# Optimization experiments

Hardware: AMD Instinct MI355X
Metric: run time of the kernel (lower is better)

Reference implementation:

```python
import jax, jax.numpy as jnp
import numpy as np

B, T, D, N = 32, 512, 1024, 1024


def setup_inputs() -> dict:
    key = jax.random.key(0)
    k1, k2, k3, k4, k5 = jax.random.split(key, 5)
    x = jax.random.normal(k1, (B, T, D), dtype=jnp.float32)
    h0 = jnp.zeros((B, N), dtype=jnp.float32)  # self.h Variable init
    # GRUCell params: gate kernel [D+N, 2N], candidate kernel [D+N, N]
    Wg = jax.random.normal(k2, (D + N, 2 * N), dtype=jnp.float32) * 0.05
    bg = jax.random.normal(k3, (2 * N,), dtype=jnp.float32) * 0.05 + 1.0  # TF gate bias init 1.0
    Wc = jax.random.normal(k4, (D + N, N), dtype=jnp.float32) * 0.05
    bc = jax.random.normal(k5, (N,), dtype=jnp.float32) * 0.05
    return {"x": x, "h0": h0, "Wg": Wg, "bg": bg, "Wc": Wc, "bc": bc}


def reference(x, h0, Wg, bg, Wc, bc):
    # tf.nn.rnn_cell.GRUCell recurrence via dynamic_rnn, single layer
    def step(h, x_t):
        xh = jnp.concatenate([x_t, h], axis=-1)           # [B, D+N]
        gates = jax.nn.sigmoid(xh @ Wg + bg)              # [B, 2N]
        r, u = jnp.split(gates, 2, axis=-1)
        xrh = jnp.concatenate([x_t, r * h], axis=-1)      # [B, D+N]
        c = jnp.tanh(xrh @ Wc + bc)                       # [B, N]
        h_new = u * h + (1.0 - u) * c
        return h_new, h_new

    xs = jnp.swapaxes(x, 0, 1)                            # [T, B, D]
    _, outs = jax.lax.scan(step, h0, xs)                  # outs: [T, B, N]
    outputs = jnp.swapaxes(outs, 0, 1)                    # [B, T, N]
    activations = outputs.reshape(-1, N)                  # [B*T, N]
    return activations
```

## Files before the change

### kernel.cpp

```cpp
#include <hip/hip_runtime.h>
#include <hip/hip_bf16.h>

#define B_ 32
#define T_ 512
#define D_ 1024
#define N_ 1024
#define NWG 192
#define NGATE 128
#define TPB 256
#define SMEM_BYTES (131072 + 8192 + 64 + 2112)

typedef __attribute__((ext_vector_type(8))) short short8v;
typedef __attribute__((ext_vector_type(4))) float f32x4;

__device__ __forceinline__ float bf2f(unsigned short u) {
  union { float f; unsigned int i; } c; c.i = ((unsigned int)u) << 16; return c.f;
}
__device__ __forceinline__ unsigned short f2bf(float f) {
  union { float f; unsigned int i; } c; c.f = f;
  unsigned int r = c.i + 0x7FFFu + ((c.i >> 16) & 1u);
  return (unsigned short)(r >> 16);
}
__device__ __forceinline__ unsigned cvtpk(float a, float b) {
  unsigned r;
  asm("v_cvt_pk_bf16_f32 %0, %1, %2" : "=v"(r) : "v"(a), "v"(b));
  return r;
}
__device__ __forceinline__ short8v pack_frag(f32x4 lo, f32x4 hi) {
  union { unsigned u[4]; short8v s; } c;
  c.u[0] = cvtpk(lo[0], lo[1]); c.u[1] = cvtpk(lo[2], lo[3]);
  c.u[2] = cvtpk(hi[0], hi[1]); c.u[3] = cvtpk(hi[2], hi[3]);
  return c.s;
}

__device__ __forceinline__ void st_bf16_sc(unsigned short* p, unsigned short v) {
  asm volatile("global_store_short %0, %1, off sc0 sc1"
               :: "v"((unsigned long long)p), "v"((unsigned)v) : "memory");
}
__device__ __forceinline__ void st_f32_sc(float* p, float v) {
  asm volatile("global_store_dword %0, %1, off sc0 sc1"
               :: "v"((unsigned long long)p), "v"(v) : "memory");
}

__device__ __forceinline__ void flag_store(unsigned* line, unsigned v) {
  __hip_atomic_store(line, v, __ATOMIC_RELAXED, __HIP_MEMORY_SCOPE_AGENT);
}
__device__ __forceinline__ void poll_pred(const unsigned* p, bool act, unsigned tgt) {
  int tries = 0;
  for (;;) {
    unsigned v = tgt;
    if (act) v = __hip_atomic_load(p, __ATOMIC_RELAXED, __HIP_MEMORY_SCOPE_AGENT);
    if (__all((int)(v >= tgt))) break;
    __builtin_amdgcn_s_sleep(1);
    if (++tries > (1 << 20)) break;
  }
}

__device__ __forceinline__ int frag_off(int m, int k) {
  const int mt = m >> 4, ks = k >> 5, kk = k & 31;
  const int l = (m & 15) + (((kk >> 2) & 3) << 4);
  const int j = (kk & 3) + ((kk >> 4) << 2);
  return ((mt * 32 + ks) * 64 + l) * 8 + j;
}

template <int KS>
__device__ __forceinline__ void build_xfrags(const float* __restrict__ x, int t,
                                             int kbase, int lane,
                                             short8v frag[2][KS]) {
#pragma unroll
  for (int mt = 0; mt < 2; ++mt) {
    const int m = mt * 16 + (lane & 15);
    const float* row = x + ((size_t)m * T_ + t) * D_;
#pragma unroll
    for (int ks = 0; ks < KS; ++ks) {
      const int k0 = kbase + ks * 32 + ((lane >> 4) << 2);
      f32x4 lo = *(const f32x4*)(row + k0);
      f32x4 hi = *(const f32x4*)(row + k0 + 16);
      frag[mt][ks] = pack_frag(lo, hi);
    }
  }
}

template <int KS>
__device__ __forceinline__ void mfma_reg(const short8v frag[2][KS],
                                         const unsigned short* __restrict__ ldsW,
                                         int ksg0, f32x4* acc, int lane) {
#pragma unroll
  for (int mt = 0; mt < 2; ++mt)
#pragma unroll
    for (int ks = 0; ks < KS; ++ks) {
      const int ksg = ksg0 + ks;
      short8v bhi = *(const short8v*)(ldsW + ((size_t)(0 * 64 + ksg) * 64 + lane) * 8);
      short8v blo = *(const short8v*)(ldsW + ((size_t)(1 * 64 + ksg) * 64 + lane) * 8);
      acc[mt] = __builtin_amdgcn_mfma_f32_16x16x32_bf16(frag[mt][ks], bhi, acc[mt], 0, 0, 0);
      acc[mt] = __builtin_amdgcn_mfma_f32_16x16x32_bf16(frag[mt][ks], blo, acc[mt], 0, 0, 0);
    }
}

__global__ __launch_bounds__(TPB, 1) void gru_persistent(
    const float* __restrict__ x, const float* __restrict__ h0,
    const float* __restrict__ Wg, const float* __restrict__ bg,
    const float* __restrict__ Wc, const float* __restrict__ bc,
    float* __restrict__ out,
    unsigned* __restrict__ ctrs,
    unsigned short* __restrict__ hq,
    unsigned short* __restrict__ rhq,
    float* __restrict__ u_buf,
    float* __restrict__ h_buf)
{
  const int wg = blockIdx.x;
  const int tid = threadIdx.x;
  const int lane = tid & 63;
  const int wv = tid >> 6;

  extern __shared__ char smem[];
  unsigned short* ldsW = (unsigned short*)smem;
  float* ldsR = (float*)(smem + 131072);
  float* ldsBias = (float*)(smem + 131072 + 8192);
  float* ldsH = (float*)(smem + 131072 + 8192 + 64);

  unsigned* flagH = ctrs;
  unsigned* flagG = ctrs + 64 * 16;

  const bool is_gate = wg < NGATE;
  const int c0 = (is_gate ? wg : (wg - NGATE)) * 16;
  const float* Wsrc = is_gate ? Wg : Wc;
  const int ldw = is_gate ? 2 * N_ : N_;
  const float* bias = is_gate ? bg : bc;

  const int col = tid & 15, row = tid >> 4;
  const int colg = c0 + col;
  const int b0 = row, b1 = 16 + row;

  for (int i = tid; i < 64 * 64; i += TPB) {
    const int ks = i >> 6, l = i & 63;
    const int n = l & 15, kqp = (l >> 4) * 4;
#pragma unroll
    for (int j = 0; j < 8; ++j) {
      const int k = ks * 32 + ((j < 4) ? 0 : 16) + kqp + (j & 3);
      const float w = Wsrc[(size_t)k * ldw + c0 + n];
      const unsigned short hi = f2bf(w);
      const unsigned short lo = f2bf(w - bf2f(hi));
      ldsW[((size_t)(0 * 64 + ks) * 64 + l) * 8 + j] = hi;
      ldsW[((size_t)(1 * 64 + ks) * 64 + l) * 8 + j] = lo;
    }
  }
  if (tid < 16) ldsBias[tid] = bias[c0 + tid];
  __syncthreads();

  if (is_gate) {
    const bool r_wg = (c0 < N_);
    unsigned* myflag = flagG + (size_t)wg * 16;
    const unsigned* pollp = nullptr; bool pact = false;
    if (lane < 16)                { pollp = flagH + (size_t)(16 * wv + lane) * 16; pact = true; }
    else if (lane == 16 && r_wg)  { pollp = flagH + (size_t)wg * 16;               pact = true; }

    f32x4 accA[2] = {{0.f,0.f,0.f,0.f},{0.f,0.f,0.f,0.f}};
    {
      short8v xf[2][8];
      build_xfrags<8>(x, 0, wv * 256, lane, xf);
      mfma_reg<8>(xf, ldsW, wv * 8, accA, lane);
    }
    for (int t = 0; t < T_; ++t) {
      poll_pred(pollp, pact, (unsigned)(t + 1));
      f32x4 hvec = {0.f,0.f,0.f,0.f};
      const bool do_h = r_wg && (tid < 128);
      if (do_h) {
        const float* hsrc = h_buf + (size_t)(c0 + (tid & 15)) * 32 + (tid >> 4) * 4;
        asm volatile("global_load_dwordx4 %0, %1, off sc0 sc1"
                     : "=v"(hvec) : "v"((unsigned long long)hsrc) : "memory");
      }
      short8v areg[2][8];
#pragma unroll
      for (int mt = 0; mt < 2; ++mt)
#pragma unroll
        for (int ks = 0; ks < 8; ++ks) {
          const unsigned short* p =
              hq + ((size_t)((mt * 32 + wv * 8 + ks) * 64 + lane)) * 8;
          asm volatile("global_load_dwordx4 %0, %1, off sc0 sc1"
                       : "=v"(areg[mt][ks]) : "v"((unsigned long long)p) : "memory");
        }
      asm volatile("s_waitcnt vmcnt(0)" ::: "memory");
      __builtin_amdgcn_sched_barrier(0);
      if (do_h) {
        float* d = ldsH + (tid & 15) * 33 + (tid >> 4) * 4;
        d[0] = hvec[0]; d[1] = hvec[1]; d[2] = hvec[2]; d[3] = hvec[3];
      }
#pragma unroll
      for (int mt = 0; mt < 2; ++mt)
#pragma unroll
        for (int ks = 0; ks < 8; ++ks) {
          const int ksg = 32 + wv * 8 + ks;
          short8v bhi = *(const short8v*)(ldsW + ((size_t)(0 * 64 + ksg) * 64 + lane) * 8);
          short8v blo = *(const short8v*)(ldsW + ((size_t)(1 * 64 + ksg) * 64 + lane) * 8);
          accA[mt] = __builtin_amdgcn_mfma_f32_16x16x32_bf16(areg[mt][ks], bhi, accA[mt], 0, 0, 0);
          accA[mt] = __builtin_amdgcn_mfma_f32_16x16x32_bf16(areg[mt][ks], blo, accA[mt], 0, 0, 0);
        }
#pragma unroll
      for (int mt = 0; mt < 2; ++mt)
#pragma unroll
        for (int r = 0; r < 4; ++r)
          ldsR[(wv * 2 + mt) * 256 + (4 * (lane >> 4) + r) * 16 + (lane & 15)] = accA[mt][r];
      __syncthreads();
      {
        float s0 = ldsR[0 * 256 + tid] + ldsR[2 * 256 + tid]
                 + ldsR[4 * 256 + tid] + ldsR[6 * 256 + tid];
        float s1 = ldsR[1 * 256 + tid] + ldsR[3 * 256 + tid]
                 + ldsR[5 * 256 + tid] + ldsR[7 * 256 + tid];
        float p0 = fminf(fmaxf(s0 + ldsBias[col], -30.f), 30.f);
        float p1 = fminf(fmaxf(s1 + ldsBias[col], -30.f), 30.f);
        const float g0 = 1.f / (1.f + __expf(-p0));
        const float g1 = 1.f / (1.f + __expf(-p1));
        if (r_wg) {
          const float hv0 = ldsH[col * 33 + row];
          const float hv1 = ldsH[col * 33 + row + 16];
          st_bf16_sc(rhq + frag_off(b0, colg), f2bf(g0 * hv0));
          st_bf16_sc(rhq + frag_off(b1, colg), f2bf(g1 * hv1));
        } else {
          st_f32_sc(u_buf + b0 * N_ + (colg - N_), g0);
          st_f32_sc(u_buf + b1 * N_ + (colg - N_), g1);
        }
      }
      asm volatile("s_waitcnt vmcnt(0)" ::: "memory");
      __syncthreads();
      if (tid == 0) flag_store(myflag, (unsigned)(t + 1));
      if (t + 1 < T_) {
        accA[0] = (f32x4){0.f,0.f,0.f,0.f};
        accA[1] = (f32x4){0.f,0.f,0.f,0.f};
        short8v xf[2][8];
        build_xfrags<8>(x, t + 1, wv * 256, lane, xf);
        mfma_reg<8>(xf, ldsW, wv * 8, accA, lane);
      }
    }
  } else {
    const int cidx = wg - NGATE;
    unsigned* myflag = flagH + (size_t)cidx * 16;
    const unsigned* p1 = nullptr; bool a1 = false;
    if (lane < 16)       { p1 = flagG + (size_t)(16 * wv + lane) * 16;  a1 = true; }
    else if (lane == 16) { p1 = flagG + (size_t)(64 + cidx) * 16;       a1 = true; }
    const unsigned* p2 = nullptr; bool a2 = false;
    if (lane < 16)       { p2 = flagG + (size_t)(64 + 16 * wv + lane) * 16; a2 = true; }

    float hreg0 = h0[b0 * N_ + colg];
    float hreg1 = h0[b1 * N_ + colg];
    st_f32_sc(h_buf + (size_t)colg * 32 + b0, hreg0);
    st_f32_sc(h_buf + (size_t)colg * 32 + b1, hreg1);
    st_bf16_sc(hq + frag_off(b0, colg), f2bf(hreg0));
    st_bf16_sc(hq + frag_off(b1, colg), f2bf(hreg1));
    asm volatile("s_waitcnt vmcnt(0)" ::: "memory");
    __syncthreads();
    if (tid == 0) flag_store(myflag, 1u);

    f32x4 accA[2] = {{0.f,0.f,0.f,0.f},{0.f,0.f,0.f,0.f}};
    {
      short8v xf[2][8];
      build_xfrags<8>(x, 0, wv * 256, lane, xf);
      mfma_reg<8>(xf, ldsW, wv * 8, accA, lane);
    }
    for (int t = 0; t < T_; ++t) {
      poll_pred(p1, a1, (unsigned)(t + 1));
      float uv0, uv1;
      asm volatile("global_load_dword %0, %2, off sc0 sc1\n\t"
                   "global_load_dword %1, %3, off sc0 sc1"
                   : "=&v"(uv0), "=&v"(uv1)
                   : "v"((unsigned long long)(u_buf + b0 * N_ + colg)),
                     "v"((unsigned long long)(u_buf + b1 * N_ + colg))
                   : "memory");
      short8v areg[2][8];
#pragma unroll
      for (int mt = 0; mt < 2; ++mt)
#pragma unroll
        for (int ks = 0; ks < 8; ++ks) {
          const unsigned short* p =
              rhq + ((size_t)((mt * 32 + wv * 8 + ks) * 64 + lane)) * 8;
          asm volatile("global_load_dwordx4 %0, %1, off sc0 sc1"
                       : "=v"(areg[mt][ks]) : "v"((unsigned long long)p) : "memory");
        }
      asm volatile("s_waitcnt vmcnt(0)" ::: "memory");
      __builtin_amdgcn_sched_barrier(0);
#pragma unroll
      for (int mt = 0; mt < 2; ++mt)
#pragma unroll
        for (int ks = 0; ks < 8; ++ks) {
          const int ksg = 32 + wv * 8 + ks;
          short8v bhi = *(const short8v*)(ldsW + ((size_t)(0 * 64 + ksg) * 64 + lane) * 8);
          short8v blo = *(const short8v*)(ldsW + ((size_t)(1 * 64 + ksg) * 64 + lane) * 8);
          accA[mt] = __builtin_amdgcn_mfma_f32_16x16x32_bf16(areg[mt][ks], bhi, accA[mt], 0, 0, 0);
          accA[mt] = __builtin_amdgcn_mfma_f32_16x16x32_bf16(areg[mt][ks], blo, accA[mt], 0, 0, 0);
        }
      poll_pred(p2, a2, (unsigned)(t + 1));
#pragma unroll
      for (int mt = 0; mt < 2; ++mt)
#pragma unroll
        for (int r = 0; r < 4; ++r)
          ldsR[(wv * 2 + mt) * 256 + (4 * (lane >> 4) + r) * 16 + (lane & 15)] = accA[mt][r];
      __syncthreads();
      {
        float s0 = ldsR[0 * 256 + tid] + ldsR[2 * 256 + tid]
                 + ldsR[4 * 256 + tid] + ldsR[6 * 256 + tid];
        float s1 = ldsR[1 * 256 + tid] + ldsR[3 * 256 + tid]
                 + ldsR[5 * 256 + tid] + ldsR[7 * 256 + tid];
        float p0 = fminf(fmaxf(s0 + ldsBias[col], -20.f), 20.f);
        float p1v = fminf(fmaxf(s1 + ldsBias[col], -20.f), 20.f);
        const float e0 = __expf(2.f * p0), e1 = __expf(2.f * p1v);
        const float c0v = (e0 - 1.f) / (e0 + 1.f);
        const float c1v = (e1 - 1.f) / (e1 + 1.f);
        const float hn0 = uv0 * hreg0 + (1.f - uv0) * c0v;
        const float hn1 = uv1 * hreg1 + (1.f - uv1) * c1v;
        hreg0 = hn0; hreg1 = hn1;
        st_bf16_sc(hq + frag_off(b0, colg), f2bf(hn0));
        st_bf16_sc(hq + frag_off(b1, colg), f2bf(hn1));
        st_f32_sc(h_buf + (size_t)colg * 32 + b0, hn0);
        st_f32_sc(h_buf + (size_t)colg * 32 + b1, hn1);
        out[((size_t)b0 * T_ + t) * N_ + colg] = hn0;
        out[((size_t)b1 * T_ + t) * N_ + colg] = hn1;
      }
      asm volatile("s_waitcnt vmcnt(0)" ::: "memory");
      __syncthreads();
      if (tid == 0) flag_store(myflag, (unsigned)(t + 2));
      if (t + 1 < T_) {
        accA[0] = (f32x4){0.f,0.f,0.f,0.f};
        accA[1] = (f32x4){0.f,0.f,0.f,0.f};
        short8v xf[2][8];
        build_xfrags<8>(x, t + 1, wv * 256, lane, xf);
        mfma_reg<8>(xf, ldsW, wv * 8, accA, lane);
      }
    }
  }
}

extern "C" void kernel_launch(void* const* d_in, const int* in_sizes, int n_in,
                              void* d_out, int out_size, void* d_ws, size_t ws_size,
                              hipStream_t stream) {
  const float* x  = (const float*)d_in[0];
  const float* h0 = (const float*)d_in[1];
  const float* Wg = (const float*)d_in[2];
  const float* bg = (const float*)d_in[3];
  const float* Wc = (const float*)d_in[4];
  const float* bc = (const float*)d_in[5];
  float* out = (float*)d_out;

  char* w = (char*)d_ws;
  unsigned* ctrs       = (unsigned*)(w + 0);
  unsigned short* hq   = (unsigned short*)(w + 16384);
  unsigned short* rhq  = (unsigned short*)(w + 81920);
  float* u_buf         = (float*)(w + 147456);
  float* h_buf         = (float*)(w + 278528);

  hipFuncSetAttribute((const void*)gru_persistent,
                      hipFuncAttributeMaxDynamicSharedMemorySize, SMEM_BYTES);
  hipMemsetAsync(w, 0, 16384, stream);
  gru_persistent<<<NWG, TPB, SMEM_BYTES, stream>>>(
      x, h0, Wg, bg, Wc, bc, out, ctrs, hq, rhq, u_buf, h_buf);
}
```

Before: 3.244 ms.

## Use per-wave completion flags and double-buffered LDS reduction to drop block barriers

Replaces the per-workgroup completion flag with one flag per wavefront, so each wave signals right after its own stores drain and the trailing __syncthreads before the flag store goes away. Consumers poll four wave flags per producer, folded into a combined two-pointer poll. The LDS reduction buffer is double-buffered by step parity so the next step can write without a barrier. h_buf moves to a [B,N] layout that gate blocks load directly, removing the LDS staging of h, and the output store is moved after the flag publish to take it off the critical path. The cost is more flag polling traffic and a larger flag region to clear with memset.

Result: slower. 3.631 ms (+11.9%).

```diff
diff --git a/kernel.cpp b/kernel.cpp
--- a/kernel.cpp
+++ b/kernel.cpp
@@ -8,7 +8,7 @@
 #define NWG 192
 #define NGATE 128
 #define TPB 256
-#define SMEM_BYTES (131072 + 8192 + 64 + 2112)
+#define SMEM_BYTES (131072 + 16384 + 64)
 
 typedef __attribute__((ext_vector_type(8))) short short8v;
 typedef __attribute__((ext_vector_type(4))) float f32x4;
@@ -45,12 +45,14 @@
 __device__ __forceinline__ void flag_store(unsigned* line, unsigned v) {
   __hip_atomic_store(line, v, __ATOMIC_RELAXED, __HIP_MEMORY_SCOPE_AGENT);
 }
-__device__ __forceinline__ void poll_pred(const unsigned* p, bool act, unsigned tgt) {
+__device__ __forceinline__ void poll2(const unsigned* p0, bool a0,
+                                      const unsigned* p1, bool a1, unsigned tgt) {
   int tries = 0;
   for (;;) {
-    unsigned v = tgt;
-    if (act) v = __hip_atomic_load(p, __ATOMIC_RELAXED, __HIP_MEMORY_SCOPE_AGENT);
-    if (__all((int)(v >= tgt))) break;
+    unsigned v0 = tgt, v1 = tgt;
+    if (a0) v0 = __hip_atomic_load(p0, __ATOMIC_RELAXED, __HIP_MEMORY_SCOPE_AGENT);
+    if (a1) v1 = __hip_atomic_load(p1, __ATOMIC_RELAXED, __HIP_MEMORY_SCOPE_AGENT);
+    if (__all((int)(v0 >= tgt && v1 >= tgt))) break;
     __builtin_amdgcn_s_sleep(1);
     if (++tries > (1 << 20)) break;
   }
@@ -116,11 +118,10 @@
   extern __shared__ char smem[];
   unsigned short* ldsW = (unsigned short*)smem;
   float* ldsR = (float*)(smem + 131072);
-  float* ldsBias = (float*)(smem + 131072 + 8192);
-  float* ldsH = (float*)(smem + 131072 + 8192 + 64);
+  float* ldsBias = (float*)(smem + 131072 + 16384);
 
   unsigned* flagH = ctrs;
-  unsigned* flagG = ctrs + 64 * 16;
+  unsigned* flagG = ctrs + 256 * 16;
 
   const bool is_gate = wg < NGATE;
   const int c0 = (is_gate ? wg : (wg - NGATE)) * 16;
@@ -150,10 +151,10 @@
 
   if (is_gate) {
     const bool r_wg = (c0 < N_);
-    unsigned* myflag = flagG + (size_t)wg * 16;
-    const unsigned* pollp = nullptr; bool pact = false;
-    if (lane < 16)                { pollp = flagH + (size_t)(16 * wv + lane) * 16; pact = true; }
-    else if (lane == 16 && r_wg)  { pollp = flagH + (size_t)wg * 16;               pact = true; }
+    unsigned* wflag = flagG + (size_t)(wg * 4 + wv) * 16;
+    const unsigned* pp = flagH + (size_t)((16 * wv + (lane >> 2)) * 4 + (lane & 3)) * 16;
+    const unsigned* pe = flagH + (size_t)(wg * 4 + wv) * 16;
+    const bool ae = r_wg && (lane == 0);
 
     f32x4 accA[2] = {{0.f,0.f,0.f,0.f},{0.f,0.f,0.f,0.f}};
     {
@@ -162,14 +163,15 @@
       mfma_reg<8>(xf, ldsW, wv * 8, accA, lane);
     }
     for (int t = 0; t < T_; ++t) {
-      poll_pred(pollp, pact, (unsigned)(t + 1));
-      f32x4 hvec = {0.f,0.f,0.f,0.f};
-      const bool do_h = r_wg && (tid < 128);
-      if (do_h) {
-        const float* hsrc = h_buf + (size_t)(c0 + (tid & 15)) * 32 + (tid >> 4) * 4;
-        asm volatile("global_load_dwordx4 %0, %1, off sc0 sc1"
-                     : "=v"(hvec) : "v"((unsigned long long)hsrc) : "memory");
-      }
+      poll2(pp, true, pe, ae, (unsigned)(t + 1));
+      float hv0 = 0.f, hv1 = 0.f;
+      if (r_wg)
+        asm volatile("global_load_dword %0, %2, off sc0 sc1\n\t"
+                     "global_load_dword %1, %3, off sc0 sc1"
+                     : "=&v"(hv0), "=&v"(hv1)
+                     : "v"((unsigned long long)(h_buf + b0 * N_ + colg)),
+                       "v"((unsigned long long)(h_buf + b1 * N_ + colg))
+                     : "memory");
       short8v areg[2][8];
 #pragma unroll
       for (int mt = 0; mt < 2; ++mt)
@@ -182,10 +184,6 @@
         }
       asm volatile("s_waitcnt vmcnt(0)" ::: "memory");
       __builtin_amdgcn_sched_barrier(0);
-      if (do_h) {
-        float* d = ldsH + (tid & 15) * 33 + (tid >> 4) * 4;
-        d[0] = hvec[0]; d[1] = hvec[1]; d[2] = hvec[2]; d[3] = hvec[3];
-      }
 #pragma unroll
       for (int mt = 0; mt < 2; ++mt)
 #pragma unroll
@@ -196,24 +194,23 @@
           accA[mt] = __builtin_amdgcn_mfma_f32_16x16x32_bf16(areg[mt][ks], bhi, accA[mt], 0, 0, 0);
           accA[mt] = __builtin_amdgcn_mfma_f32_16x16x32_bf16(areg[mt][ks], blo, accA[mt], 0, 0, 0);
         }
+      float* ldsRp = ldsR + (t & 1) * 2048;
 #pragma unroll
       for (int mt = 0; mt < 2; ++mt)
 #pragma unroll
         for (int r = 0; r < 4; ++r)
-          ldsR[(wv * 2 + mt) * 256 + (4 * (lane >> 4) + r) * 16 + (lane & 15)] = accA[mt][r];
+          ldsRp[(wv * 2 + mt) * 256 + (4 * (lane >> 4) + r) * 16 + (lane & 15)] = accA[mt][r];
       __syncthreads();
       {
-        float s0 = ldsR[0 * 256 + tid] + ldsR[2 * 256 + tid]
-                 + ldsR[4 * 256 + tid] + ldsR[6 * 256 + tid];
-        float s1 = ldsR[1 * 256 + tid] + ldsR[3 * 256 + tid]
-                 + ldsR[5 * 256 + tid] + ldsR[7 * 256 + tid];
+        float s0 = ldsRp[0 * 256 + tid] + ldsRp[2 * 256 + tid]
+                 + ldsRp[4 * 256 + tid] + ldsRp[6 * 256 + tid];
+        float s1 = ldsRp[1 * 256 + tid] + ldsRp[3 * 256 + tid]
+                 + ldsRp[5 * 256 + tid] + ldsRp[7 * 256 + tid];
         float p0 = fminf(fmaxf(s0 + ldsBias[col], -30.f), 30.f);
         float p1 = fminf(fmaxf(s1 + ldsBias[col], -30.f), 30.f);
         const float g0 = 1.f / (1.f + __expf(-p0));
         const float g1 = 1.f / (1.f + __expf(-p1));
         if (r_wg) {
-          const float hv0 = ldsH[col * 33 + row];
-          const float hv1 = ldsH[col * 33 + row + 16];
           st_bf16_sc(rhq + frag_off(b0, colg), f2bf(g0 * hv0));
           st_bf16_sc(rhq + frag_off(b1, colg), f2bf(g1 * hv1));
         } else {
@@ -222,8 +219,7 @@
         }
       }
       asm volatile("s_waitcnt vmcnt(0)" ::: "memory");
-      __syncthreads();
-      if (tid == 0) flag_store(myflag, (unsigned)(t + 1));
+      if (lane == 0) flag_store(wflag, (unsigned)(t + 1));
       if (t + 1 < T_) {
         accA[0] = (f32x4){0.f,0.f,0.f,0.f};
         accA[1] = (f32x4){0.f,0.f,0.f,0.f};
@@ -234,22 +230,20 @@
     }
   } else {
     const int cidx = wg - NGATE;
-    unsigned* myflag = flagH + (size_t)cidx * 16;
-    const unsigned* p1 = nullptr; bool a1 = false;
-    if (lane < 16)       { p1 = flagG + (size_t)(16 * wv + lane) * 16;  a1 = true; }
-    else if (lane == 16) { p1 = flagG + (size_t)(64 + cidx) * 16;       a1 = true; }
-    const unsigned* p2 = nullptr; bool a2 = false;
-    if (lane < 16)       { p2 = flagG + (size_t)(64 + 16 * wv + lane) * 16; a2 = true; }
+    unsigned* wflag = flagH + (size_t)(cidx * 4 + wv) * 16;
+    const unsigned* pp1 = flagG + (size_t)((16 * wv + (lane >> 2)) * 4 + (lane & 3)) * 16;
+    const unsigned* pe1 = flagG + (size_t)((64 + cidx) * 4 + (lane & 3)) * 16;
+    const bool ae1 = (lane < 4);
+    const unsigned* pp2 = flagG + (size_t)((64 + 16 * wv + (lane >> 2)) * 4 + (lane & 3)) * 16;
 
     float hreg0 = h0[b0 * N_ + colg];
     float hreg1 = h0[b1 * N_ + colg];
-    st_f32_sc(h_buf + (size_t)colg * 32 + b0, hreg0);
-    st_f32_sc(h_buf + (size_t)colg * 32 + b1, hreg1);
+    st_f32_sc(h_buf + b0 * N_ + colg, hreg0);
+    st_f32_sc(h_buf + b1 * N_ + colg, hreg1);
     st_bf16_sc(hq + frag_off(b0, colg), f2bf(hreg0));
     st_bf16_sc(hq + frag_off(b1, colg), f2bf(hreg1));
     asm volatile("s_waitcnt vmcnt(0)" ::: "memory");
-    __syncthreads();
-    if (tid == 0) flag_store(myflag, 1u);
+    if (lane == 0) flag_store(wflag, 1u);
 
     f32x4 accA[2] = {{0.f,0.f,0.f,0.f},{0.f,0.f,0.f,0.f}};
     {
@@ -258,7 +252,7 @@
       mfma_reg<8>(xf, ldsW, wv * 8, accA, lane);
     }
     for (int t = 0; t < T_; ++t) {
-      poll_pred(p1, a1, (unsigned)(t + 1));
+      poll2(pp1, true, pe1, ae1, (unsigned)(t + 1));
       float uv0, uv1;
       asm volatile("global_load_dword %0, %2, off sc0 sc1\n\t"
                    "global_load_dword %1, %3, off sc0 sc1"
@@ -288,36 +282,37 @@
           accA[mt] = __builtin_amdgcn_mfma_f32_16x16x32_bf16(areg[mt][ks], bhi, accA[mt], 0, 0, 0);
           accA[mt] = __builtin_amdgcn_mfma_f32_16x16x32_bf16(areg[mt][ks], blo, accA[mt], 0, 0, 0);
         }
-      poll_pred(p2, a2, (unsigned)(t + 1));
+      poll2(pp2, true, nullptr, false, (unsigned)(t + 1));
+      float* ldsRp = ldsR + (t & 1) * 2048;
 #pragma unroll
       for (int mt = 0; mt < 2; ++mt)
 #pragma unroll
         for (int r = 0; r < 4; ++r)
-          ldsR[(wv * 2 + mt) * 256 + (4 * (lane >> 4) + r) * 16 + (lane & 15)] = accA[mt][r];
+          ldsRp[(wv * 2 + mt) * 256 + (4 * (lane >> 4) + r) * 16 + (lane & 15)] = accA[mt][r];
       __syncthreads();
+      float hn0, hn1;
       {
-        float s0 = ldsR[0 * 256 + tid] + ldsR[2 * 256 + tid]
-                 + ldsR[4 * 256 + tid] + ldsR[6 * 256 + tid];
-        float s1 = ldsR[1 * 256 + tid] + ldsR[3 * 256 + tid]
-                 + ldsR[5 * 256 + tid] + ldsR[7 * 256 + tid];
+        float s0 = ldsRp[0 * 256 + tid] + ldsRp[2 * 256 + tid]
+                 + ldsRp[4 * 256 + tid] + ldsRp[6 * 256 + tid];
+        float s1 = ldsRp[1 * 256 + tid] + ldsRp[3 * 256 + tid]
+                 + ldsRp[5 * 256 + tid] + ldsRp[7 * 256 + tid];
         float p0 = fminf(fmaxf(s0 + ldsBias[col], -20.f), 20.f);
         float p1v = fminf(fmaxf(s1 + ldsBias[col], -20.f), 20.f);
         const float e0 = __expf(2.f * p0), e1 = __expf(2.f * p1v);
         const float c0v = (e0 - 1.f) / (e0 + 1.f);
         const float c1v = (e1 - 1.f) / (e1 + 1.f);
-        const float hn0 = uv0 * hreg0 + (1.f - uv0) * c0v;
-        const float hn1 = uv1 * hreg1 + (1.f - uv1) * c1v;
+        hn0 = uv0 * hreg0 + (1.f - uv0) * c0v;
+        hn1 = uv1 * hreg1 + (1.f - uv1) * c1v;
         hreg0 = hn0; hreg1 = hn1;
         st_bf16_sc(hq + frag_off(b0, colg), f2bf(hn0));
         st_bf16_sc(hq + frag_off(b1, colg), f2bf(hn1));
-        st_f32_sc(h_buf + (size_t)colg * 32 + b0, hn0);
-        st_f32_sc(h_buf + (size_t)colg * 32 + b1, hn1);
-        out[((size_t)b0 * T_ + t) * N_ + colg] = hn0;
-        out[((size_t)b1 * T_ + t) * N_ + colg] = hn1;
+        st_f32_sc(h_buf + b0 * N_ + colg, hn0);
+        st_f32_sc(h_buf + b1 * N_ + colg, hn1);
       }
       asm volatile("s_waitcnt vmcnt(0)" ::: "memory");
-      __syncthreads();
-      if (tid == 0) flag_store(myflag, (unsigned)(t + 2));
+      if (lane == 0) flag_store(wflag, (unsigned)(t + 2));
+      out[((size_t)b0 * T_ + t) * N_ + colg] = hn0;
+      out[((size_t)b1 * T_ + t) * N_ + colg] = hn1;
       if (t + 1 < T_) {
         accA[0] = (f32x4){0.f,0.f,0.f,0.f};
         accA[1] = (f32x4){0.f,0.f,0.f,0.f};
@@ -342,14 +337,14 @@
 
   char* w = (char*)d_ws;
   unsigned* ctrs       = (unsigned*)(w + 0);
-  unsigned short* hq   = (unsigned short*)(w + 16384);
-  unsigned short* rhq  = (unsigned short*)(w + 81920);
-  float* u_buf         = (float*)(w + 147456);
-  float* h_buf         = (float*)(w + 278528);
+  unsigned short* hq   = (unsigned short*)(w + 49152);
+  unsigned short* rhq  = (unsigned short*)(w + 114688);
+  float* u_buf         = (float*)(w + 180224);
+  float* h_buf         = (float*)(w + 311296);
 
   hipFuncSetAttribute((const void*)gru_persistent,
                       hipFuncAttributeMaxDynamicSharedMemorySize, SMEM_BYTES);
-  hipMemsetAsync(w, 0, 16384, stream);
+  hipMemsetAsync(w, 0, 49152, stream);
   gru_persistent<<<NWG, TPB, SMEM_BYTES, stream>>>(
       x, h0, Wg, bg, Wc, bc, out, ctrs, hq, rhq, u_buf, h_buf);
 }
```
